# Kernel optimization log

Measured on AMD Instinct MI355X. Metric: run time of the kernel, lower is better.

## Reference

```python
import jax, jax.numpy as jnp
import numpy as np

N_NODES = 300000
N_EDGES = 1200000
D = 128
B = 1000
VOCAB = 26  # vocab_size + 1


def setup_inputs() -> dict:
    key = jax.random.key(0)
    ks = jax.random.split(key, 10)
    x = jax.random.randint(ks[0], (N_NODES,), 0, VOCAB, dtype=jnp.int32)
    edge_index = jax.random.randint(ks[1], (2, N_EDGES), 0, N_NODES, dtype=jnp.int32)
    # cumulative protein boundaries: B proteins of equal length, last entry == N_NODES
    amino_acids_numbers = (jnp.arange(1, B + 1, dtype=jnp.int32) * (N_NODES // B))
    s = 1.0 / np.sqrt(D)
    emb = jax.random.normal(ks[2], (VOCAB, D), dtype=jnp.float32)
    W_rel1 = jax.random.uniform(ks[3], (D, D), jnp.float32, -s, s)
    b_rel1 = jax.random.uniform(ks[4], (D,), jnp.float32, -s, s)
    W_root1 = jax.random.uniform(ks[5], (D, D), jnp.float32, -s, s)
    W_rel2 = jax.random.uniform(ks[6], (D, D), jnp.float32, -s, s)
    b_rel2 = jax.random.uniform(ks[7], (D,), jnp.float32, -s, s)
    W_root2 = jax.random.uniform(ks[8], (D, D), jnp.float32, -s, s)
    return {"x": x, "edge_index": edge_index, "amino_acids_numbers": amino_acids_numbers,
            "emb": emb, "W_rel1": W_rel1, "b_rel1": b_rel1, "W_root1": W_root1,
            "W_rel2": W_rel2, "b_rel2": b_rel2, "W_root2": W_root2}


def _graph_conv(nodes, src, tgt, W_rel, b_rel, W_root, n):
    # PyG GraphConv (aggr='add'): out = Lin_rel(sum_{j->i} x_j) + Lin_root(x_i)
    agg = jax.ops.segment_sum(nodes[src], tgt, num_segments=n)  # [N, D]
    return agg @ W_rel.T + b_rel + nodes @ W_root.T


def reference(x, edge_index, amino_acids_numbers, emb,
              W_rel1, b_rel1, W_root1, W_rel2, b_rel2, W_root2):
    n = x.shape[0]
    src, tgt = edge_index[0], edge_index[1]
    nodes = emb[x]  # [N, D] embedding lookup
    nodes = _graph_conv(nodes, src, tgt, W_rel1, b_rel1, W_root1, n)
    nodes = _graph_conv(nodes, src, tgt, W_rel2, b_rel2, W_root2, n)
    # segment mean pooling over [start:end) slices defined by cumulative ends
    ends = amino_acids_numbers
    seg = jnp.searchsorted(ends, jnp.arange(n), side='right')  # node -> protein id
    b = ends.shape[0]
    sums = jax.ops.segment_sum(nodes, seg, num_segments=b)  # [B, D]
    counts = jnp.diff(ends, prepend=jnp.zeros((1,), ends.dtype)).astype(nodes.dtype)
    return sums / counts[:, None]
```

## Files before the change

kernel.cpp:

```cpp
#include <hip/hip_runtime.h>

#define DD 128
#define VV 26
#define NW 13
#define CS4 4
#define G 256
#define TWIN 512
#define PAD 4096

__device__ __forceinline__ unsigned wsum(unsigned v) {
#pragma unroll
    for (int m = 32; m >= 1; m >>= 1) v += __shfl_xor(v, m, 64);
    return v;
}

__device__ __forceinline__ int wscan_incl(int v) {
    int lane = threadIdx.x & 63;
#pragma unroll
    for (int off = 1; off < 64; off <<= 1) {
        int t = __shfl_up(v, off, 64);
        if (lane >= off) v += t;
    }
    return v;
}

__device__ __forceinline__ int seg_guess(const int* ends, int B, int t, int Lavg) {
    int p = t / Lavg;
    if (p > B - 1) p = B - 1;
    while (p > 0 && ends[p - 1] > t) --p;
    while (ends[p] <= t) ++p;
    return p;
}

__device__ __forceinline__ int bseg(const int* cumx, int j) {
    int lo = 0, hi = G - 1;
    while (lo < hi) {
        int mid = (lo + hi + 1) >> 1;
        if (cumx[mid] <= j) lo = mid; else hi = mid - 1;
    }
    return lo;
}

__global__ __launch_bounds__(1024)
void k_sort_pre(const int* __restrict__ src, const int* __restrict__ tgt,
                const int* __restrict__ x, const int* __restrict__ ends,
                int E, int B, int chunk, int Lavg,
                const float* __restrict__ emb,
                const float* __restrict__ W1r, const float* __restrict__ b1,
                const float* __restrict__ W1o,
                const float* __restrict__ W2r, const float* __restrict__ W2o,
                unsigned long long* __restrict__ sorted_ts,
                int* __restrict__ segstartT, int* __restrict__ seghistT,
                float* __restrict__ P1, float* __restrict__ P2,
                float* __restrict__ P3, float* __restrict__ uvec,
                float* __restrict__ wvec) {
    extern __shared__ char smem[];
    int tid = threadIdx.x;
    int chunkp = (chunk + 1) & ~1;

    if (blockIdx.x >= G) {
        float* e1r = (float*)smem;
        float* r1r = e1r + DD;
        float* b1s = r1r + DD;
        int v = blockIdx.x - G;
        int d = tid;
        if (d < DD) {
            const float* e = emb + v * DD;
            const float* w1r = W1r + d * DD;
            const float* w1o = W1o + d * DD;
            float s1 = 0.f, s2 = 0.f;
            for (int k = 0; k < DD; ++k) { float ev = e[k]; s1 += ev * w1r[k]; s2 += ev * w1o[k]; }
            e1r[d] = s1; r1r[d] = s2; b1s[d] = b1[d];
        }
        __syncthreads();
        if (d < DD) {
            const float* wr = W2r + d * DD;
            const float* wo = W2o + d * DD;
            float p1 = 0.f, p2 = 0.f, p3 = 0.f, su = 0.f, sw = 0.f;
            for (int k = 0; k < DD; ++k) {
                float a = wr[k], bb = wo[k], ee = e1r[k], r = r1r[k], c = b1s[k];
                p1 += ee * a; p2 += r * a + ee * bb; p3 += r * bb;
                su += c * a; sw += c * bb;
            }
            P1[v * DD + d] = p1; P2[v * DD + d] = p2; P3[v * DD + d] = p3;
            if (v == 0) { uvec[d] = su; wvec[d] = sw; }
        }
        return;
    }

    unsigned long long* pay = (unsigned long long*)smem;
    int* lds_ends = (int*)(pay + chunk);
    int* hist = lds_ends + 1024;
    int* cur = hist + 1024;
    int* wsums = cur + 1024;
    unsigned short* lpe = (unsigned short*)(wsums + 16);

    int b = blockIdx.x;
    int e0 = b * chunk;
    int e1 = min(E, e0 + chunk);
    int clen = e1 - e0;

    for (int i = tid; i < B; i += 1024) lds_ends[i] = ends[i];
    hist[tid] = 0;
    __syncthreads();

    for (int i = tid; i < clen; i += 1024) {
        int t = tgt[e0 + i];
        int p = seg_guess(lds_ends, B, t, Lavg);
        atomicAdd(&hist[p], 1);
        lpe[i] = (unsigned short)p;
    }
    __syncthreads();

    int v = hist[tid];
    if (tid < B) seghistT[tid * G + b] = v;
    int wave = tid >> 6, lane = tid & 63;
    int incl = wscan_incl(v);
    if (lane == 63) wsums[wave] = incl;
    __syncthreads();
    int offw = 0;
    for (int w = 0; w < wave; ++w) offw += wsums[w];
    int excl = incl + offw - v;
    if (tid < B) {
        cur[tid] = excl;
        segstartT[tid * G + b] = e0 + excl;
    }
    __syncthreads();

    for (int i = tid; i < clen; i += 1024) {
        int e = e0 + i;
        int p = lpe[i];
        int s = src[e];
        int t = tgt[e];
        int lbl = x[s];
        int pst = (p == 0) ? 0 : lds_ends[p - 1];
        int pos = atomicAdd(&cur[p], 1);
        pay[pos] = ((unsigned long long)(unsigned)s << 16)
                 | (unsigned long long)(unsigned)(((t - pst) << 5) | lbl);
    }
    __syncthreads();

    for (int i = tid; i < clen; i += 1024) sorted_ts[e0 + i] = pay[i];
}

__global__ __launch_bounds__(256)
void k_counts(const int* __restrict__ ends,
              const int* __restrict__ seghistT, const int* __restrict__ segstartT,
              int B, int E, const unsigned long long* __restrict__ sorted_ts,
              unsigned* __restrict__ counts, unsigned* __restrict__ csG,
              int* __restrict__ DpG) {
    __shared__ unsigned tab[TWIN * CS4];
    __shared__ int cumx[G + 4], segb[G], wsums[4];
    int p = blockIdx.x, tid = threadIdx.x;
    int wave = tid >> 6, lane = tid & 63;
    int start = (p == 0) ? 0 : ends[p - 1];
    int end = ends[p];
    int Lp = end - start;

    int h = seghistT[p * G + tid];
    segb[tid] = segstartT[p * G + tid];
    int incl = wscan_incl(h);
    if (lane == 63) wsums[wave] = incl;
    __syncthreads();
    int offw = 0;
    for (int w = 0; w < wave; ++w) offw += wsums[w];
    cumx[tid] = incl + offw - h;
    if (tid == 255) { cumx[G] = incl + offw; DpG[p] = incl + offw; }
    __syncthreads();
    int Dp = cumx[G];

    for (int w0 = 0; w0 < Lp; w0 += TWIN) {
        int wlen = min(TWIN, Lp - w0);
        __syncthreads();
        for (int i = tid; i < wlen * CS4; i += 256) tab[i] = 0u;
        __syncthreads();
        for (int j = tid; j < Dp; j += 256) {
            int bb = bseg(cumx, j);
            int pos = segb[bb] + (j - cumx[bb]);
            unsigned long long ts = sorted_ts[pos];
            unsigned tl = (unsigned)(ts & 0xFFFFull);
            if (w0 == 0) csG[(size_t)p * PAD + j] = (unsigned)(ts >> 16);
            int lbl = (int)(tl & 31u);
            int tloc = (int)(tl >> 5) - w0;
            if ((unsigned)tloc < (unsigned)wlen)
                atomicAdd(&tab[tloc * CS4 + (lbl >> 3)], 1u << ((lbl & 7) * 4));
        }
        __syncthreads();
        unsigned* dst = counts + ((size_t)(start + w0)) * CS4;
        for (int i = tid; i < wlen * CS4; i += 256) dst[i] = tab[i];
    }
}

__global__ __launch_bounds__(256)
void k_protein(const int* __restrict__ x, const int* __restrict__ ends,
               const int* __restrict__ DpG, const unsigned* __restrict__ csG,
               const unsigned* __restrict__ counts,
               const float* __restrict__ P1, const float* __restrict__ P2,
               const float* __restrict__ P3, const float* __restrict__ uvec,
               const float* __restrict__ wvec, const float* __restrict__ b2,
               int B, int E, float* __restrict__ out) {
    __shared__ unsigned red[4][48];
    __shared__ float c2f[VV], cpf[VV], hpf[VV];
    int p = blockIdx.x, tid = threadIdx.x;
    int wave = tid >> 6, lane = tid & 63;
    int start = (p == 0) ? 0 : ends[p - 1];
    int end = ends[p];
    int Dp = DpG[p];

    unsigned c2[16], cp[16], hpw[NW];
#pragma unroll
    for (int k = 0; k < 16; ++k) { c2[k] = 0u; cp[k] = 0u; }
#pragma unroll
    for (int w = 0; w < NW; ++w) hpw[w] = 0u;

    const unsigned* cs = csG + (size_t)p * PAD;
    for (int j = tid; j < Dp; j += 256) {
        int s = (int)cs[j];
        uint4 c0 = *reinterpret_cast<const uint4*>(counts + (size_t)s * CS4);
        unsigned w;
        w = c0.x; c2[0]  += w & 0x000F000Fu; c2[1]  += (w >> 4) & 0x000F000Fu;
                  c2[2]  += (w >> 8) & 0x000F000Fu; c2[3]  += (w >> 12) & 0x000F000Fu;
        w = c0.y; c2[4]  += w & 0x000F000Fu; c2[5]  += (w >> 4) & 0x000F000Fu;
                  c2[6]  += (w >> 8) & 0x000F000Fu; c2[7]  += (w >> 12) & 0x000F000Fu;
        w = c0.z; c2[8]  += w & 0x000F000Fu; c2[9]  += (w >> 4) & 0x000F000Fu;
                  c2[10] += (w >> 8) & 0x000F000Fu; c2[11] += (w >> 12) & 0x000F000Fu;
        w = c0.w; c2[12] += w & 0x000F000Fu; c2[13] += (w >> 4) & 0x000F000Fu;
                  c2[14] += (w >> 8) & 0x000F000Fu; c2[15] += (w >> 12) & 0x000F000Fu;
    }

    for (int i = start + tid; i < end; i += 256) {
        uint4 c0 = *reinterpret_cast<const uint4*>(counts + (size_t)i * CS4);
        unsigned w;
        w = c0.x; cp[0]  += w & 0x000F000Fu; cp[1]  += (w >> 4) & 0x000F000Fu;
                  cp[2]  += (w >> 8) & 0x000F000Fu; cp[3]  += (w >> 12) & 0x000F000Fu;
        w = c0.y; cp[4]  += w & 0x000F000Fu; cp[5]  += (w >> 4) & 0x000F000Fu;
                  cp[6]  += (w >> 8) & 0x000F000Fu; cp[7]  += (w >> 12) & 0x000F000Fu;
        w = c0.z; cp[8]  += w & 0x000F000Fu; cp[9]  += (w >> 4) & 0x000F000Fu;
                  cp[10] += (w >> 8) & 0x000F000Fu; cp[11] += (w >> 12) & 0x000F000Fu;
        w = c0.w; cp[12] += w & 0x000F000Fu; cp[13] += (w >> 4) & 0x000F000Fu;
                  cp[14] += (w >> 8) & 0x000F000Fu; cp[15] += (w >> 12) & 0x000F000Fu;
        int l = x[i];
        unsigned inc = 1u << ((l & 1) * 16);
        int wi = l >> 1;
#pragma unroll
        for (int w2 = 0; w2 < NW; ++w2) hpw[w2] += (w2 == wi) ? inc : 0u;
    }

#pragma unroll
    for (int k = 0; k < 16; ++k) {
        unsigned a = wsum(c2[k]); if (lane == 0) red[wave][k] = a;
        unsigned b = wsum(cp[k]); if (lane == 0) red[wave][16 + k] = b;
    }
#pragma unroll
    for (int w = 0; w < NW; ++w) {
        unsigned a = wsum(hpw[w]); if (lane == 0) red[wave][32 + w] = a;
    }
    __syncthreads();
    if (tid < 45) {
        unsigned t = red[0][tid] + red[1][tid] + red[2][tid] + red[3][tid];
        if (tid < 32) {
            int i = tid & 15;
            int base = 8 * (i >> 2) + (i & 3);
            float* dst = (tid < 16) ? c2f : cpf;
            if (base < VV) dst[base] = (float)(t & 0xFFFFu);
            if (base + 4 < VV) dst[base + 4] = (float)(t >> 16);
        } else {
            int w = tid - 32;
            hpf[w * 2] = (float)(t & 0xFFFFu);
            if (w * 2 + 1 < VV) hpf[w * 2 + 1] = (float)(t >> 16);
        }
    }
    __syncthreads();

    if (tid < DD) {
        int d = tid;
        float acc = 0.f;
#pragma unroll
        for (int v = 0; v < VV; ++v)
            acc += c2f[v] * P1[v * DD + d] + cpf[v] * P2[v * DD + d] + hpf[v] * P3[v * DD + d];
        float Lp = (float)(end - start);
        float invL = 1.f / Lp;
        float Dpf = (float)Dp;
        out[(size_t)p * DD + d] = acc * invL + (Dpf * invL) * uvec[d] + wvec[d] + b2[d];
    }
}

extern "C" void kernel_launch(void* const* d_in, const int* in_sizes, int n_in,
                              void* d_out, int out_size, void* d_ws, size_t ws_size,
                              hipStream_t stream) {
    const int*   x       = (const int*)d_in[0];
    const int*   edge    = (const int*)d_in[1];
    const int*   ends    = (const int*)d_in[2];
    const float* emb     = (const float*)d_in[3];
    const float* W_rel1  = (const float*)d_in[4];
    const float* b_rel1  = (const float*)d_in[5];
    const float* W_root1 = (const float*)d_in[6];
    const float* W_rel2  = (const float*)d_in[7];
    const float* b_rel2  = (const float*)d_in[8];
    const float* W_root2 = (const float*)d_in[9];

    const int N = in_sizes[0];
    const int E = in_sizes[1] / 2;
    const int B = in_sizes[2];
    const int Lavg = (N / B) > 0 ? (N / B) : 1;
    const int chunk = (E + G - 1) / G;
    const int chunkp = (chunk + 1) & ~1;

    const int* srcp = edge;
    const int* tgtp = edge + E;

    auto align256 = [](size_t v) { return (v + 255) & ~(size_t)255; };
    char* ws = (char*)d_ws;
    size_t off = 0;
    unsigned* counts = (unsigned*)(ws + off);                 off += align256((size_t)N * CS4 * 4);
    int* segstartT = (int*)(ws + off);                        off += align256((size_t)B * G * 4);
    int* seghistT = (int*)(ws + off);                         off += align256((size_t)B * G * 4);
    int* DpG = (int*)(ws + off);                              off += align256((size_t)B * 4);
    unsigned long long* sorted_ts = (unsigned long long*)(ws + off); off += align256((size_t)E * 8);
    unsigned* csG = (unsigned*)(ws + off);                    off += align256((size_t)B * PAD * 4);
    float* P1 = (float*)(ws + off);                           off += align256((size_t)VV * DD * 4);
    float* P2 = (float*)(ws + off);                           off += align256((size_t)VV * DD * 4);
    float* P3 = (float*)(ws + off);                           off += align256((size_t)VV * DD * 4);
    float* uvec = (float*)(ws + off);                         off += align256((size_t)DD * 4);
    float* wvec = (float*)(ws + off);                         off += align256((size_t)DD * 4);
    (void)ws_size; (void)n_in; (void)out_size;


    size_t ldsb = (size_t)chunk * 8 + (size_t)(3 * 1024 + 16) * 4 + (size_t)chunkp * 2;
    k_sort_pre<<<G + VV, 1024, ldsb, stream>>>(
        srcp, tgtp, x, ends, E, B, chunk, Lavg,
        emb, W_rel1, b_rel1, W_root1, W_rel2, W_root2,
        sorted_ts, segstartT, seghistT, P1, P2, P3, uvec, wvec);

    k_counts<<<B, 256, 0, stream>>>(ends, seghistT, segstartT, B, E, sorted_ts,
                                    counts, csG, DpG);

    k_protein<<<B, 256, 0, stream>>>(x, ends, DpG, csG, counts,
                                     P1, P2, P3, uvec, wvec, b_rel2, B, E, (float*)d_out);
}
```

Measured before the change: 64.66 us.

## Scatter sorted payload directly to global and compute per-protein count sums in k_counts

The sort kernel no longer stages the bucketed payload in LDS before copying it out. It writes each packed edge record straight to its global position, which shrinks dynamic LDS and drops a barrier and a copy loop, but the global writes become scattered. The per-protein sum of node label counts (cp) is now reduced inside k_counts from the LDS tab it already holds and stored in a small CpG buffer. k_protein then reads 26 floats instead of re-reading the protein's rows of counts from global memory.

```diff
diff --git a/kernel.cpp b/kernel.cpp
--- a/kernel.cpp
+++ b/kernel.cpp
@@ -88,8 +88,7 @@
         return;
     }
 
-    unsigned long long* pay = (unsigned long long*)smem;
-    int* lds_ends = (int*)(pay + chunk);
+    int* lds_ends = (int*)smem;
     int* hist = lds_ends + 1024;
     int* cur = hist + 1024;
     int* wsums = cur + 1024;
@@ -135,12 +134,9 @@
         int lbl = x[s];
         int pst = (p == 0) ? 0 : lds_ends[p - 1];
         int pos = atomicAdd(&cur[p], 1);
-        pay[pos] = ((unsigned long long)(unsigned)s << 16)
-                 | (unsigned long long)(unsigned)(((t - pst) << 5) | lbl);
-    }
-    __syncthreads();
-
-    for (int i = tid; i < clen; i += 1024) sorted_ts[e0 + i] = pay[i];
+        sorted_ts[e0 + pos] = ((unsigned long long)(unsigned)s << 16)
+                            | (unsigned long long)(unsigned)(((t - pst) << 5) | lbl);
+    }
 }
 
 __global__ __launch_bounds__(256)
@@ -148,9 +144,10 @@
               const int* __restrict__ seghistT, const int* __restrict__ segstartT,
               int B, int E, const unsigned long long* __restrict__ sorted_ts,
               unsigned* __restrict__ counts, unsigned* __restrict__ csG,
-              int* __restrict__ DpG) {
+              int* __restrict__ DpG, float* __restrict__ CpG) {
     __shared__ unsigned tab[TWIN * CS4];
     __shared__ int cumx[G + 4], segb[G], wsums[4];
+    __shared__ unsigned red[4][16];
     int p = blockIdx.x, tid = threadIdx.x;
     int wave = tid >> 6, lane = tid & 63;
     int start = (p == 0) ? 0 : ends[p - 1];
@@ -168,6 +165,10 @@
     if (tid == 255) { cumx[G] = incl + offw; DpG[p] = incl + offw; }
     __syncthreads();
     int Dp = cumx[G];
+
+    unsigned cp[16];
+#pragma unroll
+    for (int k = 0; k < 16; ++k) cp[k] = 0u;
 
     for (int w0 = 0; w0 < Lp; w0 += TWIN) {
         int wlen = min(TWIN, Lp - w0);
@@ -188,18 +189,42 @@
         __syncthreads();
         unsigned* dst = counts + ((size_t)(start + w0)) * CS4;
         for (int i = tid; i < wlen * CS4; i += 256) dst[i] = tab[i];
+        for (int r = tid; r < wlen; r += 256) {
+            uint4 c0 = *reinterpret_cast<const uint4*>(&tab[r * CS4]);
+            unsigned w;
+            w = c0.x; cp[0]  += w & 0x000F000Fu; cp[1]  += (w >> 4) & 0x000F000Fu;
+                      cp[2]  += (w >> 8) & 0x000F000Fu; cp[3]  += (w >> 12) & 0x000F000Fu;
+            w = c0.y; cp[4]  += w & 0x000F000Fu; cp[5]  += (w >> 4) & 0x000F000Fu;
+                      cp[6]  += (w >> 8) & 0x000F000Fu; cp[7]  += (w >> 12) & 0x000F000Fu;
+            w = c0.z; cp[8]  += w & 0x000F000Fu; cp[9]  += (w >> 4) & 0x000F000Fu;
+                      cp[10] += (w >> 8) & 0x000F000Fu; cp[11] += (w >> 12) & 0x000F000Fu;
+            w = c0.w; cp[12] += w & 0x000F000Fu; cp[13] += (w >> 4) & 0x000F000Fu;
+                      cp[14] += (w >> 8) & 0x000F000Fu; cp[15] += (w >> 12) & 0x000F000Fu;
+        }
+    }
+
+#pragma unroll
+    for (int k = 0; k < 16; ++k) {
+        unsigned a = wsum(cp[k]); if (lane == 0) red[wave][k] = a;
+    }
+    __syncthreads();
+    if (tid < 16) {
+        unsigned t = red[0][tid] + red[1][tid] + red[2][tid] + red[3][tid];
+        int base = 8 * (tid >> 2) + (tid & 3);
+        if (base < VV) CpG[(size_t)p * VV + base] = (float)(t & 0xFFFFu);
+        if (base + 4 < VV) CpG[(size_t)p * VV + base + 4] = (float)(t >> 16);
     }
 }
 
 __global__ __launch_bounds__(256)
 void k_protein(const int* __restrict__ x, const int* __restrict__ ends,
                const int* __restrict__ DpG, const unsigned* __restrict__ csG,
-               const unsigned* __restrict__ counts,
+               const unsigned* __restrict__ counts, const float* __restrict__ CpG,
                const float* __restrict__ P1, const float* __restrict__ P2,
                const float* __restrict__ P3, const float* __restrict__ uvec,
                const float* __restrict__ wvec, const float* __restrict__ b2,
                int B, int E, float* __restrict__ out) {
-    __shared__ unsigned red[4][48];
+    __shared__ unsigned red[4][32];
     __shared__ float c2f[VV], cpf[VV], hpf[VV];
     int p = blockIdx.x, tid = threadIdx.x;
     int wave = tid >> 6, lane = tid & 63;
@@ -207,9 +232,11 @@
     int end = ends[p];
     int Dp = DpG[p];
 
-    unsigned c2[16], cp[16], hpw[NW];
-#pragma unroll
-    for (int k = 0; k < 16; ++k) { c2[k] = 0u; cp[k] = 0u; }
+    if (tid < VV) cpf[tid] = CpG[(size_t)p * VV + tid];
+
+    unsigned c2[16], hpw[NW];
+#pragma unroll
+    for (int k = 0; k < 16; ++k) c2[k] = 0u;
 #pragma unroll
     for (int w = 0; w < NW; ++w) hpw[w] = 0u;
 
@@ -229,16 +256,6 @@
     }
 
     for (int i = start + tid; i < end; i += 256) {
-        uint4 c0 = *reinterpret_cast<const uint4*>(counts + (size_t)i * CS4);
-        unsigned w;
-        w = c0.x; cp[0]  += w & 0x000F000Fu; cp[1]  += (w >> 4) & 0x000F000Fu;
-                  cp[2]  += (w >> 8) & 0x000F000Fu; cp[3]  += (w >> 12) & 0x000F000Fu;
-        w = c0.y; cp[4]  += w & 0x000F000Fu; cp[5]  += (w >> 4) & 0x000F000Fu;
-                  cp[6]  += (w >> 8) & 0x000F000Fu; cp[7]  += (w >> 12) & 0x000F000Fu;
-        w = c0.z; cp[8]  += w & 0x000F000Fu; cp[9]  += (w >> 4) & 0x000F000Fu;
-                  cp[10] += (w >> 8) & 0x000F000Fu; cp[11] += (w >> 12) & 0x000F000Fu;
-        w = c0.w; cp[12] += w & 0x000F000Fu; cp[13] += (w >> 4) & 0x000F000Fu;
-                  cp[14] += (w >> 8) & 0x000F000Fu; cp[15] += (w >> 12) & 0x000F000Fu;
         int l = x[i];
         unsigned inc = 1u << ((l & 1) * 16);
         int wi = l >> 1;
@@ -249,23 +266,20 @@
 #pragma unroll
     for (int k = 0; k < 16; ++k) {
         unsigned a = wsum(c2[k]); if (lane == 0) red[wave][k] = a;
-        unsigned b = wsum(cp[k]); if (lane == 0) red[wave][16 + k] = b;
     }
 #pragma unroll
     for (int w = 0; w < NW; ++w) {
-        unsigned a = wsum(hpw[w]); if (lane == 0) red[wave][32 + w] = a;
-    }
-    __syncthreads();
-    if (tid < 45) {
+        unsigned a = wsum(hpw[w]); if (lane == 0) red[wave][16 + w] = a;
+    }
+    __syncthreads();
+    if (tid < 16 + NW) {
         unsigned t = red[0][tid] + red[1][tid] + red[2][tid] + red[3][tid];
-        if (tid < 32) {
-            int i = tid & 15;
-            int base = 8 * (i >> 2) + (i & 3);
-            float* dst = (tid < 16) ? c2f : cpf;
-            if (base < VV) dst[base] = (float)(t & 0xFFFFu);
-            if (base + 4 < VV) dst[base + 4] = (float)(t >> 16);
+        if (tid < 16) {
+            int base = 8 * (tid >> 2) + (tid & 3);
+            if (base < VV) c2f[base] = (float)(t & 0xFFFFu);
+            if (base + 4 < VV) c2f[base + 4] = (float)(t >> 16);
         } else {
-            int w = tid - 32;
+            int w = tid - 16;
             hpf[w * 2] = (float)(t & 0xFFFFu);
             if (w * 2 + 1 < VV) hpf[w * 2 + 1] = (float)(t >> 16);
         }
@@ -318,6 +332,7 @@
     int* DpG = (int*)(ws + off);                              off += align256((size_t)B * 4);
     unsigned long long* sorted_ts = (unsigned long long*)(ws + off); off += align256((size_t)E * 8);
     unsigned* csG = (unsigned*)(ws + off);                    off += align256((size_t)B * PAD * 4);
+    float* CpG = (float*)(ws + off);                          off += align256((size_t)B * VV * 4);
     float* P1 = (float*)(ws + off);                           off += align256((size_t)VV * DD * 4);
     float* P2 = (float*)(ws + off);                           off += align256((size_t)VV * DD * 4);
     float* P3 = (float*)(ws + off);                           off += align256((size_t)VV * DD * 4);
@@ -326,15 +341,15 @@
     (void)ws_size; (void)n_in; (void)out_size;
 
 
-    size_t ldsb = (size_t)chunk * 8 + (size_t)(3 * 1024 + 16) * 4 + (size_t)chunkp * 2;
+    size_t ldsb = (size_t)(3 * 1024 + 16) * 4 + (size_t)chunkp * 2;
     k_sort_pre<<<G + VV, 1024, ldsb, stream>>>(
         srcp, tgtp, x, ends, E, B, chunk, Lavg,
         emb, W_rel1, b_rel1, W_root1, W_rel2, W_root2,
         sorted_ts, segstartT, seghistT, P1, P2, P3, uvec, wvec);
 
     k_counts<<<B, 256, 0, stream>>>(ends, seghistT, segstartT, B, E, sorted_ts,
-                                    counts, csG, DpG);
-
-    k_protein<<<B, 256, 0, stream>>>(x, ends, DpG, csG, counts,
+                                    counts, csG, DpG, CpG);
+
+    k_protein<<<B, 256, 0, stream>>>(x, ends, DpG, csG, counts, CpG,
                                      P1, P2, P3, uvec, wvec, b_rel2, B, E, (float*)d_out);
 }
```

After: 69.12 us. 6.9% more time.
